# Kernel optimization log

Measured on AMD Instinct MI355X. Metric: run time of the kernel, lower is better.

## Reference

```python
import jax, jax.numpy as jnp
import numpy as np

N, K, D, H = 10000, 30, 128, 4
DH = D // H
E = N * K

def setup_inputs() -> dict:
    ks = jax.random.split(jax.random.key(0), 12)
    s = 0.05
    h = jax.random.normal(ks[0], (N, D), jnp.float32)
    e = jax.random.normal(ks[1], (E, D), jnp.float32)
    # edges grouped by source node, K neighbors each (required by the (i j) rearranges)
    src = jnp.repeat(jnp.arange(N, dtype=jnp.int32), K)
    dst = jax.random.randint(ks[2], (E,), 0, N, dtype=jnp.int32)
    edge_index = jnp.stack([src, dst], axis=0)
    return {
        'h': h, 'e': e, 'edge_index': edge_index,
        'att_w1': jax.random.normal(ks[3], (3 * D, D)) * s, 'att_b1': jnp.zeros((D,)),
        'att_w2': jax.random.normal(ks[4], (D, D)) * s,     'att_b2': jnp.zeros((D,)),
        'att_w3': jax.random.normal(ks[5], (D, H)) * s,     'att_b3': jnp.zeros((H,)),
        'node_w1': jax.random.normal(ks[6], (2 * D, D)) * s, 'node_b1': jnp.zeros((D,)),
        'node_w2': jax.random.normal(ks[7], (D, D)) * s,     'node_b2': jnp.zeros((D,)),
        'node_w3': jax.random.normal(ks[8], (D, D)) * s,     'node_b3': jnp.zeros((D,)),
        'to_h_w': jax.random.normal(ks[9], (D, D)) * s,
    }

def reference(h, e, edge_index, att_w1, att_b1, att_w2, att_b2, att_w3, att_b3,
              node_w1, node_b1, node_w2, node_b2, node_w3, node_b3, to_h_w):
    gelu = lambda x: jax.nn.gelu(x, approximate=False)  # torch nn.GELU default (erf)
    hi = h[edge_index[0]]                               # [E, D] gather
    hj = h[edge_index[1]]                               # [E, D] gather
    hi_eij_hj = jnp.concatenate([hi, e, hj], axis=-1)   # [E, 3D]
    eij_hj = jnp.concatenate([e, hj], axis=-1)          # [E, 2D]
    # attention logits per head
    w = jax.nn.relu(hi_eij_hj @ att_w1 + att_b1)
    w = jax.nn.relu(w @ att_w2 + att_b2)
    w = (w @ att_w3 + att_b3).reshape(N, K, H)          # (i j) h -> i j h
    w = w / jnp.sqrt(jnp.float32(DH))
    att = jax.nn.softmax(w, axis=1)                     # softmax over neighbors j
    # values per edge, split per head
    v = gelu(eij_hj @ node_w1 + node_b1)
    v = gelu(v @ node_w2 + node_b2)
    v = (v @ node_w3 + node_b3).reshape(N, K, H, DH)    # (i j) (h d) -> i j h d
    out = jnp.einsum('nkh,nkhd->nhd', att, v).reshape(N, D)  # weighted aggregation
    return out @ to_h_w
```

## Files before the change

kernel.cpp:

```cpp
#include <hip/hip_runtime.h>
#include <hip/hip_bf16.h>

#define N_NODES 10000
#define KNEI    30
#define DIM     128
#define EDGES   (N_NODES * KNEI)

typedef __attribute__((ext_vector_type(4))) float  f32x4;
typedef __attribute__((ext_vector_type(8))) __bf16 bf16x8;
typedef __attribute__((ext_vector_type(4))) __bf16 bf16x4;

#define OFF_AW1 0
#define OFF_AW2 49152
#define OFF_NW1 65536
#define OFF_NW2 98304
#define OFF_NW3 114688
#define OFF_TH  131072
#define TOT_TILES 288
#define YHI_BYTE_OFF (300 * 1024)

__global__ __launch_bounds__(256) void repack_all(
    const float* __restrict__ aw1, const float* __restrict__ aw2,
    const float* __restrict__ nw1, const float* __restrict__ nw2,
    const float* __restrict__ nw3, const float* __restrict__ thw,
    __bf16* __restrict__ dst) {
    int t = blockIdx.x * 256 + threadIdx.x;
    if (t >= TOT_TILES * 512) return;
    int tile = t >> 9;
    int i    = t & 7;
    int lane = (t >> 3) & 63;
    const float* src; int lt;
    if      (tile < 96)  { src = aw1; lt = tile; }
    else if (tile < 128) { src = aw2; lt = tile - 96; }
    else if (tile < 192) { src = nw1; lt = tile - 128; }
    else if (tile < 224) { src = nw2; lt = tile - 192; }
    else if (tile < 256) { src = nw3; lt = tile - 224; }
    else                 { src = thw; lt = tile - 256; }
    int nt = lt & 7;
    int kt = lt >> 3;
    int k = kt * 32 + ((lane >> 4) << 3) + i;
    int n = nt * 16 + (lane & 15);
    dst[t] = (__bf16)src[k * DIM + n];
}

__device__ __forceinline__ float gelu_f(float x) {
    float u = 0.7978845608f * (x + 0.044715f * x * x * x);
    float t = 1.f - 2.f / (__expf(2.f * u) + 1.f);
    return 0.5f * x * (1.f + t);
}

__device__ __forceinline__ bf16x4 cvt4(float4 v) {
    bf16x4 r;
    r[0] = (__bf16)v.x; r[1] = (__bf16)v.y; r[2] = (__bf16)v.z; r[3] = (__bf16)v.w;
    return r;
}

__device__ __forceinline__ void mm_lds(f32x4 acc[2], const __bf16* __restrict__ wfrag,
                                       const __bf16* x, int sx, int nkt,
                                       int wv, int lane) {
    const int mrow = lane & 15;
    const int kgrp = (lane >> 4) & 3;
#pragma unroll
    for (int kt = 0; kt < nkt; ++kt) {
        bf16x8 a = *reinterpret_cast<const bf16x8*>(wfrag + ((kt * 8 + wv) * 64 + lane) * 8);
        const int kb = kt * 32 + kgrp * 8;
#pragma unroll
        for (int mf = 0; mf < 2; ++mf) {
            bf16x8 b = *reinterpret_cast<const bf16x8*>(x + (mf * 16 + mrow) * sx + kb);
            acc[mf] = __builtin_amdgcn_mfma_f32_16x16x32_bf16(a, b, acc[mf], 0, 0, 0);
        }
    }
}

__device__ __forceinline__ void store_act(f32x4 acc[2], const float* __restrict__ bias,
                                          __bf16* y, int sy, int actmode,
                                          int wv, int lane) {
    const int mrow = lane & 15;
    const int kgrp = (lane >> 4) & 3;
    const int nb = wv * 16 + kgrp * 4;
    float b0 = bias[nb], b1 = bias[nb + 1], b2 = bias[nb + 2], b3 = bias[nb + 3];
#pragma unroll
    for (int mf = 0; mf < 2; ++mf) {
        bf16x4 pk;
        float vv[4] = {acc[mf][0] + b0, acc[mf][1] + b1, acc[mf][2] + b2, acc[mf][3] + b3};
#pragma unroll
        for (int r = 0; r < 4; ++r) {
            float v = vv[r];
            v = actmode == 0 ? fmaxf(v, 0.f) : gelu_f(v);
            pk[r] = (__bf16)v;
        }
        *reinterpret_cast<bf16x4*>(y + (mf * 16 + mrow) * sy + nb) = pk;
    }
}

#define ZERO2(A) do { A[0] = (f32x4){0.f,0.f,0.f,0.f}; A[1] = (f32x4){0.f,0.f,0.f,0.f}; } while (0)

__global__ __launch_bounds__(512) void mm128(const float* __restrict__ in,
                                             float* __restrict__ outp,
                                             const __bf16* __restrict__ wfrag,
                                             const float* __restrict__ bias) {
    __shared__ __bf16 sP[64 * 136];
    const int tid  = threadIdx.x;
    const int wv   = tid >> 6;
    const int lane = tid & 63;
    const int mrow = lane & 15;
    const int kgrp = lane >> 4;
    const int base = blockIdx.x * 64;

#pragma unroll
    for (int c = 0; c < 4; ++c) {
        int idx = c * 512 + tid;
        int m  = idx >> 5;
        int jv = idx & 31;
        int row = base + m;
        float4 v = make_float4(0.f, 0.f, 0.f, 0.f);
        if (row < N_NODES) v = *reinterpret_cast<const float4*>(in + (long)row * DIM + jv * 4);
        *reinterpret_cast<bf16x4*>(&sP[m * 136 + jv * 4]) = cvt4(v);
    }
    __syncthreads();

    f32x4 acc[4];
#pragma unroll
    for (int mf = 0; mf < 4; ++mf) acc[mf] = (f32x4){0.f, 0.f, 0.f, 0.f};
#pragma unroll
    for (int kt = 0; kt < 4; ++kt) {
        bf16x8 a = *reinterpret_cast<const bf16x8*>(wfrag + ((kt * 8 + wv) * 64 + lane) * 8);
        const int kb = kt * 32 + kgrp * 8;
#pragma unroll
        for (int mf = 0; mf < 4; ++mf) {
            bf16x8 b = *reinterpret_cast<const bf16x8*>(sP + (mf * 16 + mrow) * 136 + kb);
            acc[mf] = __builtin_amdgcn_mfma_f32_16x16x32_bf16(a, b, acc[mf], 0, 0, 0);
        }
    }
    const int nb = wv * 16 + kgrp * 4;
    float b0 = 0.f, b1 = 0.f, b2 = 0.f, b3 = 0.f;
    if (bias) { b0 = bias[nb]; b1 = bias[nb + 1]; b2 = bias[nb + 2]; b3 = bias[nb + 3]; }
#pragma unroll
    for (int mf = 0; mf < 4; ++mf) {
        int row = base + mf * 16 + mrow;
        if (row < N_NODES) {
            float4 o = make_float4(acc[mf][0] + b0, acc[mf][1] + b1,
                                   acc[mf][2] + b2, acc[mf][3] + b3);
            *reinterpret_cast<float4*>(outp + (long)row * DIM + nb) = o;
        }
    }
}

__global__ __launch_bounds__(512, 4) void gnn_fused(
    const float* __restrict__ h, const float* __restrict__ e, const int* __restrict__ eidx,
    const float* __restrict__ yhi,
    const float* __restrict__ ab2, const float* __restrict__ aw3, const float* __restrict__ ab3,
    const float* __restrict__ nb1, const float* __restrict__ nb2, const float* __restrict__ nb3,
    const __bf16* __restrict__ wp, float* __restrict__ pre_out) {

    __shared__ __bf16 S[32 * 264];
    __shared__ __bf16 Y1[32 * 136];
    __shared__ __bf16 Y2[32 * 136];
    __shared__ float  sLogW[8][32][4];
    __shared__ float  sW[32][4];

    const int tid  = threadIdx.x;
    const int wv   = tid >> 6;
    const int lane = tid & 63;
    const int mrow = lane & 15;
    const int kg   = (lane >> 4) & 3;
    const int node = blockIdx.x;
    const long ebase = (long)node * KNEI;

#pragma unroll
    for (int c = 0; c < 2; ++c) {
        int idx = c * 512 + tid;
        int m  = idx >> 5;
        int jv = idx & 31;
        float4 ev = make_float4(0.f, 0.f, 0.f, 0.f), hjv = ev;
        if (m < KNEI) {
            long ge = ebase + m;
            ev  = *reinterpret_cast<const float4*>(e + ge * DIM + jv * 4);
            int dstn = eidx[EDGES + ge];
            hjv = *reinterpret_cast<const float4*>(h + (long)dstn * DIM + jv * 4);
        }
        *reinterpret_cast<bf16x4*>(&S[m * 264 + jv * 4])       = cvt4(ev);
        *reinterpret_cast<bf16x4*>(&S[m * 264 + 128 + jv * 4]) = cvt4(hjv);
    }
    __syncthreads();

    f32x4 acc[2];

    ZERO2(acc);
    mm_lds(acc, wp + OFF_AW1 + 16384, S, 264, 8, wv, lane);
    store_act(acc, yhi + (long)node * DIM, Y1, 136, 0, wv, lane);
    __syncthreads();

    {
        ZERO2(acc);
        mm_lds(acc, wp + OFF_AW2, Y1, 136, 4, wv, lane);
        const int nb = wv * 16 + kg * 4;
        float b0 = ab2[nb], b1 = ab2[nb + 1], b2 = ab2[nb + 2], b3 = ab2[nb + 3];
        float4 w3v[4];
#pragma unroll
        for (int r = 0; r < 4; ++r)
            w3v[r] = *reinterpret_cast<const float4*>(aw3 + (nb + r) * 4);
        float lp[2][4];
#pragma unroll
        for (int mf = 0; mf < 2; ++mf) {
            lp[mf][0] = lp[mf][1] = lp[mf][2] = lp[mf][3] = 0.f;
            float vv[4] = {acc[mf][0] + b0, acc[mf][1] + b1, acc[mf][2] + b2, acc[mf][3] + b3};
#pragma unroll
            for (int r = 0; r < 4; ++r) {
                float v = fmaxf(vv[r], 0.f);
                lp[mf][0] += v * w3v[r].x;
                lp[mf][1] += v * w3v[r].y;
                lp[mf][2] += v * w3v[r].z;
                lp[mf][3] += v * w3v[r].w;
            }
        }
#pragma unroll
        for (int mf = 0; mf < 2; ++mf)
#pragma unroll
            for (int hh = 0; hh < 4; ++hh) {
                lp[mf][hh] += __shfl_xor(lp[mf][hh], 16);
                lp[mf][hh] += __shfl_xor(lp[mf][hh], 32);
            }
        if (kg == 0 && lane < 16) {
#pragma unroll
            for (int mf = 0; mf < 2; ++mf) {
                float4 o = make_float4(lp[mf][0], lp[mf][1], lp[mf][2], lp[mf][3]);
                *reinterpret_cast<float4*>(&sLogW[wv][mf * 16 + mrow][0]) = o;
            }
        }
    }
    ZERO2(acc);
    mm_lds(acc, wp + OFF_NW1, S, 264, 8, wv, lane);
    store_act(acc, nb1, Y2, 136, 1, wv, lane);
    __syncthreads();

    if (tid < 128) {
        int m = tid >> 2, hh = tid & 3;
        float s = ab3[hh];
#pragma unroll
        for (int w = 0; w < 8; ++w) s += sLogW[w][m][hh];
        sLogW[0][m][hh] = s * 0.17677669529f;
    }
    ZERO2(acc);
    mm_lds(acc, wp + OFF_NW2, Y2, 136, 4, wv, lane);
    store_act(acc, nb2, Y1, 136, 1, wv, lane);
    __syncthreads();

    ZERO2(acc);
    mm_lds(acc, wp + OFF_NW3, Y1, 136, 4, wv, lane);
    if (wv == 0 && lane < 32) {
        float4 lg = (lane < KNEI) ? *reinterpret_cast<float4*>(&sLogW[0][lane][0])
                                  : make_float4(-1e30f, -1e30f, -1e30f, -1e30f);
        float4 mx = lg;
#pragma unroll
        for (int msk = 1; msk <= 16; msk <<= 1) {
            mx.x = fmaxf(mx.x, __shfl_xor(mx.x, msk));
            mx.y = fmaxf(mx.y, __shfl_xor(mx.y, msk));
            mx.z = fmaxf(mx.z, __shfl_xor(mx.z, msk));
            mx.w = fmaxf(mx.w, __shfl_xor(mx.w, msk));
        }
        float4 ex = make_float4(__expf(lg.x - mx.x), __expf(lg.y - mx.y),
                                __expf(lg.z - mx.z), __expf(lg.w - mx.w));
        float4 sm = ex;
#pragma unroll
        for (int msk = 1; msk <= 16; msk <<= 1) {
            sm.x += __shfl_xor(sm.x, msk);
            sm.y += __shfl_xor(sm.y, msk);
            sm.z += __shfl_xor(sm.z, msk);
            sm.w += __shfl_xor(sm.w, msk);
        }
        float4 w = make_float4(ex.x / sm.x, ex.y / sm.y, ex.z / sm.z, ex.w / sm.w);
        *reinterpret_cast<float4*>(&sW[lane][0]) = w;
    }
    __syncthreads();

    {
        const int hh = wv >> 1;
        float wgt0 = sW[mrow][hh];
        float wgt1 = sW[16 + mrow][hh];
        float part[4];
#pragma unroll
        for (int r = 0; r < 4; ++r)
            part[r] = wgt0 * acc[0][r] + wgt1 * acc[1][r];
#pragma unroll
        for (int msk = 1; msk <= 8; msk <<= 1)
#pragma unroll
            for (int r = 0; r < 4; ++r)
                part[r] += __shfl_xor(part[r], msk);
        if (mrow == 0) {
            const int nb = wv * 16 + kg * 4;
            float4 o = make_float4(part[0] + nb3[nb],     part[1] + nb3[nb + 1],
                                   part[2] + nb3[nb + 2], part[3] + nb3[nb + 3]);
            *reinterpret_cast<float4*>(pre_out + (long)node * DIM + nb) = o;
        }
    }
}

extern "C" void kernel_launch(void* const* d_in, const int* in_sizes, int n_in,
                              void* d_out, int out_size, void* d_ws, size_t ws_size,
                              hipStream_t stream) {
    const float* h   = (const float*)d_in[0];
    const float* e   = (const float*)d_in[1];
    const int*   ei  = (const int*)d_in[2];
    const float* aw1 = (const float*)d_in[3];
    const float* ab1 = (const float*)d_in[4];
    const float* aw2 = (const float*)d_in[5];
    const float* ab2 = (const float*)d_in[6];
    const float* aw3 = (const float*)d_in[7];
    const float* ab3 = (const float*)d_in[8];
    const float* nw1 = (const float*)d_in[9];
    const float* nb1 = (const float*)d_in[10];
    const float* nw2 = (const float*)d_in[11];
    const float* nb2 = (const float*)d_in[12];
    const float* nw3 = (const float*)d_in[13];
    const float* nb3 = (const float*)d_in[14];
    const float* thw = (const float*)d_in[15];
    float* out = (float*)d_out;
    __bf16* wp = (__bf16*)d_ws;
    float* yhi = (float*)((char*)d_ws + YHI_BYTE_OFF);

    repack_all<<<TOT_TILES * 2, 256, 0, stream>>>(aw1, aw2, nw1, nw2, nw3, thw, wp);

    const int nblk = (N_NODES + 63) / 64;
    mm128<<<nblk, 512, 0, stream>>>(h, yhi, wp + OFF_AW1, ab1);

    gnn_fused<<<N_NODES, 512, 0, stream>>>(h, e, ei, yhi, ab2, aw3, ab3,
                                           nb1, nb2, nb3, wp, out);
    mm128<<<nblk, 512, 0, stream>>>(out, out, wp + OFF_TH, nullptr);
}
```

Measured before the change: 179.6 us.

## Merge first-layer GEMMs, split attention/value second layers across wave halves

The first-layer attention and node GEMMs now share one loop over the staged input tile, so each B fragment is loaded from LDS once and feeds both weight sets. The second layers run concurrently: waves 0-3 compute the attention layer-2 logits while waves 4-7 compute the value layer-2 GELU output into the reused S buffer. This removes one barrier stage and lets the two branches overlap instead of running back to back. The softmax is rewritten for a single wave with reciprocal instructions, and the GELU tanh form is simplified to x*sigmoid-style arithmetic with rcp. Each wave now holds more accumulators in the second layer, which may raise register pressure.

```diff
diff --git a/kernel.cpp b/kernel.cpp
--- a/kernel.cpp
+++ b/kernel.cpp
@@ -44,32 +44,15 @@
 }
 
 __device__ __forceinline__ float gelu_f(float x) {
-    float u = 0.7978845608f * (x + 0.044715f * x * x * x);
-    float t = 1.f - 2.f / (__expf(2.f * u) + 1.f);
-    return 0.5f * x * (1.f + t);
+    float y = x * fmaf(0.0713548163f, x * x, 1.5957691216f);
+    float r = __builtin_amdgcn_rcpf(__expf(y) + 1.f);
+    return x - x * r;
 }
 
 __device__ __forceinline__ bf16x4 cvt4(float4 v) {
     bf16x4 r;
     r[0] = (__bf16)v.x; r[1] = (__bf16)v.y; r[2] = (__bf16)v.z; r[3] = (__bf16)v.w;
     return r;
-}
-
-__device__ __forceinline__ void mm_lds(f32x4 acc[2], const __bf16* __restrict__ wfrag,
-                                       const __bf16* x, int sx, int nkt,
-                                       int wv, int lane) {
-    const int mrow = lane & 15;
-    const int kgrp = (lane >> 4) & 3;
-#pragma unroll
-    for (int kt = 0; kt < nkt; ++kt) {
-        bf16x8 a = *reinterpret_cast<const bf16x8*>(wfrag + ((kt * 8 + wv) * 64 + lane) * 8);
-        const int kb = kt * 32 + kgrp * 8;
-#pragma unroll
-        for (int mf = 0; mf < 2; ++mf) {
-            bf16x8 b = *reinterpret_cast<const bf16x8*>(x + (mf * 16 + mrow) * sx + kb);
-            acc[mf] = __builtin_amdgcn_mfma_f32_16x16x32_bf16(a, b, acc[mf], 0, 0, 0);
-        }
-    }
 }
 
 __device__ __forceinline__ void store_act(f32x4 acc[2], const float* __restrict__ bias,
@@ -156,7 +139,7 @@
     __shared__ __bf16 S[32 * 264];
     __shared__ __bf16 Y1[32 * 136];
     __shared__ __bf16 Y2[32 * 136];
-    __shared__ float  sLogW[8][32][4];
+    __shared__ float  sLP[4][32][4];
     __shared__ float  sW[32][4];
 
     const int tid  = threadIdx.x;
@@ -184,34 +167,66 @@
     }
     __syncthreads();
 
-    f32x4 acc[2];
-
-    ZERO2(acc);
-    mm_lds(acc, wp + OFF_AW1 + 16384, S, 264, 8, wv, lane);
-    store_act(acc, yhi + (long)node * DIM, Y1, 136, 0, wv, lane);
-    __syncthreads();
-
     {
-        ZERO2(acc);
-        mm_lds(acc, wp + OFF_AW2, Y1, 136, 4, wv, lane);
-        const int nb = wv * 16 + kg * 4;
-        float b0 = ab2[nb], b1 = ab2[nb + 1], b2 = ab2[nb + 2], b3 = ab2[nb + 3];
-        float4 w3v[4];
-#pragma unroll
-        for (int r = 0; r < 4; ++r)
-            w3v[r] = *reinterpret_cast<const float4*>(aw3 + (nb + r) * 4);
+        f32x4 aa[2], an[2];
+        ZERO2(aa); ZERO2(an);
+        const __bf16* wA = wp + OFF_AW1 + 16384;
+        const __bf16* wN = wp + OFF_NW1;
+#pragma unroll
+        for (int kt = 0; kt < 8; ++kt) {
+            const int kb = kt * 32 + kg * 8;
+            bf16x8 b0 = *reinterpret_cast<const bf16x8*>(S + mrow * 264 + kb);
+            bf16x8 b1 = *reinterpret_cast<const bf16x8*>(S + (16 + mrow) * 264 + kb);
+            bf16x8 a0 = *reinterpret_cast<const bf16x8*>(wA + ((kt * 8 + wv) * 64 + lane) * 8);
+            aa[0] = __builtin_amdgcn_mfma_f32_16x16x32_bf16(a0, b0, aa[0], 0, 0, 0);
+            aa[1] = __builtin_amdgcn_mfma_f32_16x16x32_bf16(a0, b1, aa[1], 0, 0, 0);
+            bf16x8 a1 = *reinterpret_cast<const bf16x8*>(wN + ((kt * 8 + wv) * 64 + lane) * 8);
+            an[0] = __builtin_amdgcn_mfma_f32_16x16x32_bf16(a1, b0, an[0], 0, 0, 0);
+            an[1] = __builtin_amdgcn_mfma_f32_16x16x32_bf16(a1, b1, an[1], 0, 0, 0);
+        }
+        store_act(aa, yhi + (long)node * DIM, Y1, 136, 0, wv, lane);
+        store_act(an, nb1, Y2, 136, 1, wv, lane);
+    }
+    __syncthreads();
+
+    if (wv < 4) {
+        f32x4 acc[2][2];
+        ZERO2(acc[0]); ZERO2(acc[1]);
+#pragma unroll
+        for (int kt = 0; kt < 4; ++kt) {
+            const int kb = kt * 32 + kg * 8;
+            bf16x8 b0 = *reinterpret_cast<const bf16x8*>(Y1 + mrow * 136 + kb);
+            bf16x8 b1 = *reinterpret_cast<const bf16x8*>(Y1 + (16 + mrow) * 136 + kb);
+#pragma unroll
+            for (int j = 0; j < 2; ++j) {
+                bf16x8 a = *reinterpret_cast<const bf16x8*>(wp + OFF_AW2 + (size_t)((kt * 8 + wv * 2 + j) * 64 + lane) * 8);
+                acc[j][0] = __builtin_amdgcn_mfma_f32_16x16x32_bf16(a, b0, acc[j][0], 0, 0, 0);
+                acc[j][1] = __builtin_amdgcn_mfma_f32_16x16x32_bf16(a, b1, acc[j][1], 0, 0, 0);
+            }
+        }
         float lp[2][4];
-#pragma unroll
-        for (int mf = 0; mf < 2; ++mf) {
-            lp[mf][0] = lp[mf][1] = lp[mf][2] = lp[mf][3] = 0.f;
-            float vv[4] = {acc[mf][0] + b0, acc[mf][1] + b1, acc[mf][2] + b2, acc[mf][3] + b3};
-#pragma unroll
-            for (int r = 0; r < 4; ++r) {
-                float v = fmaxf(vv[r], 0.f);
-                lp[mf][0] += v * w3v[r].x;
-                lp[mf][1] += v * w3v[r].y;
-                lp[mf][2] += v * w3v[r].z;
-                lp[mf][3] += v * w3v[r].w;
+        lp[0][0]=lp[0][1]=lp[0][2]=lp[0][3]=0.f;
+        lp[1][0]=lp[1][1]=lp[1][2]=lp[1][3]=0.f;
+#pragma unroll
+        for (int j = 0; j < 2; ++j) {
+            const int f = wv * 32 + j * 16 + kg * 4;
+            float b0 = ab2[f], b1 = ab2[f + 1], b2 = ab2[f + 2], b3 = ab2[f + 3];
+            float4 w3v[4];
+#pragma unroll
+            for (int r = 0; r < 4; ++r)
+                w3v[r] = *reinterpret_cast<const float4*>(aw3 + (f + r) * 4);
+#pragma unroll
+            for (int mf = 0; mf < 2; ++mf) {
+                float vv[4] = {acc[j][mf][0] + b0, acc[j][mf][1] + b1,
+                               acc[j][mf][2] + b2, acc[j][mf][3] + b3};
+#pragma unroll
+                for (int r = 0; r < 4; ++r) {
+                    float v = fmaxf(vv[r], 0.f);
+                    lp[mf][0] += v * w3v[r].x;
+                    lp[mf][1] += v * w3v[r].y;
+                    lp[mf][2] += v * w3v[r].z;
+                    lp[mf][3] += v * w3v[r].w;
+                }
             }
         }
 #pragma unroll
@@ -221,56 +236,75 @@
                 lp[mf][hh] += __shfl_xor(lp[mf][hh], 16);
                 lp[mf][hh] += __shfl_xor(lp[mf][hh], 32);
             }
-        if (kg == 0 && lane < 16) {
+        if (lane < 16) {
 #pragma unroll
             for (int mf = 0; mf < 2; ++mf) {
                 float4 o = make_float4(lp[mf][0], lp[mf][1], lp[mf][2], lp[mf][3]);
-                *reinterpret_cast<float4*>(&sLogW[wv][mf * 16 + mrow][0]) = o;
-            }
-        }
-    }
-    ZERO2(acc);
-    mm_lds(acc, wp + OFF_NW1, S, 264, 8, wv, lane);
-    store_act(acc, nb1, Y2, 136, 1, wv, lane);
-    __syncthreads();
-
-    if (tid < 128) {
-        int m = tid >> 2, hh = tid & 3;
-        float s = ab3[hh];
-#pragma unroll
-        for (int w = 0; w < 8; ++w) s += sLogW[w][m][hh];
-        sLogW[0][m][hh] = s * 0.17677669529f;
-    }
-    ZERO2(acc);
-    mm_lds(acc, wp + OFF_NW2, Y2, 136, 4, wv, lane);
-    store_act(acc, nb2, Y1, 136, 1, wv, lane);
-    __syncthreads();
-
-    ZERO2(acc);
-    mm_lds(acc, wp + OFF_NW3, Y1, 136, 4, wv, lane);
-    if (wv == 0 && lane < 32) {
-        float4 lg = (lane < KNEI) ? *reinterpret_cast<float4*>(&sLogW[0][lane][0])
-                                  : make_float4(-1e30f, -1e30f, -1e30f, -1e30f);
-        float4 mx = lg;
-#pragma unroll
-        for (int msk = 1; msk <= 16; msk <<= 1) {
-            mx.x = fmaxf(mx.x, __shfl_xor(mx.x, msk));
-            mx.y = fmaxf(mx.y, __shfl_xor(mx.y, msk));
-            mx.z = fmaxf(mx.z, __shfl_xor(mx.z, msk));
-            mx.w = fmaxf(mx.w, __shfl_xor(mx.w, msk));
-        }
-        float4 ex = make_float4(__expf(lg.x - mx.x), __expf(lg.y - mx.y),
-                                __expf(lg.z - mx.z), __expf(lg.w - mx.w));
-        float4 sm = ex;
-#pragma unroll
-        for (int msk = 1; msk <= 16; msk <<= 1) {
-            sm.x += __shfl_xor(sm.x, msk);
-            sm.y += __shfl_xor(sm.y, msk);
-            sm.z += __shfl_xor(sm.z, msk);
-            sm.w += __shfl_xor(sm.w, msk);
-        }
-        float4 w = make_float4(ex.x / sm.x, ex.y / sm.y, ex.z / sm.z, ex.w / sm.w);
-        *reinterpret_cast<float4*>(&sW[lane][0]) = w;
+                *reinterpret_cast<float4*>(&sLP[wv][mf * 16 + mrow][0]) = o;
+            }
+        }
+    } else {
+        const int w4 = wv - 4;
+        f32x4 acc[2][2];
+        ZERO2(acc[0]); ZERO2(acc[1]);
+#pragma unroll
+        for (int kt = 0; kt < 4; ++kt) {
+            const int kb = kt * 32 + kg * 8;
+            bf16x8 b0 = *reinterpret_cast<const bf16x8*>(Y2 + mrow * 136 + kb);
+            bf16x8 b1 = *reinterpret_cast<const bf16x8*>(Y2 + (16 + mrow) * 136 + kb);
+#pragma unroll
+            for (int j = 0; j < 2; ++j) {
+                bf16x8 a = *reinterpret_cast<const bf16x8*>(wp + OFF_NW2 + (size_t)((kt * 8 + w4 * 2 + j) * 64 + lane) * 8);
+                acc[j][0] = __builtin_amdgcn_mfma_f32_16x16x32_bf16(a, b0, acc[j][0], 0, 0, 0);
+                acc[j][1] = __builtin_amdgcn_mfma_f32_16x16x32_bf16(a, b1, acc[j][1], 0, 0, 0);
+            }
+        }
+#pragma unroll
+        for (int j = 0; j < 2; ++j) {
+            const int f = w4 * 32 + j * 16 + kg * 4;
+            float b0 = nb2[f], b1 = nb2[f + 1], b2 = nb2[f + 2], b3 = nb2[f + 3];
+#pragma unroll
+            for (int mf = 0; mf < 2; ++mf) {
+                float vv[4] = {acc[j][mf][0] + b0, acc[j][mf][1] + b1,
+                               acc[j][mf][2] + b2, acc[j][mf][3] + b3};
+                bf16x4 pk;
+#pragma unroll
+                for (int r = 0; r < 4; ++r) pk[r] = (__bf16)gelu_f(vv[r]);
+                *reinterpret_cast<bf16x4*>(S + (mf * 16 + mrow) * 136 + f) = pk;
+            }
+        }
+    }
+    __syncthreads();
+
+    if (wv == 0) {
+        const int m0 = lane >> 2, hh = lane & 3;
+        const float sc = 0.17677669529f;
+        float v0 = ab3[hh], v1 = ab3[hh];
+#pragma unroll
+        for (int w = 0; w < 4; ++w) { v0 += sLP[w][m0][hh]; v1 += sLP[w][16 + m0][hh]; }
+        v0 *= sc; v1 *= sc;
+        if (16 + m0 >= KNEI) v1 = -1e30f;
+        float mx = fmaxf(v0, v1);
+#pragma unroll
+        for (int msk = 4; msk <= 32; msk <<= 1) mx = fmaxf(mx, __shfl_xor(mx, msk));
+        float e0 = __expf(v0 - mx), e1 = __expf(v1 - mx);
+        float sm = e0 + e1;
+#pragma unroll
+        for (int msk = 4; msk <= 32; msk <<= 1) sm += __shfl_xor(sm, msk);
+        float inv = __builtin_amdgcn_rcpf(sm);
+        sW[m0][hh]      = e0 * inv;
+        sW[16 + m0][hh] = e1 * inv;
+    }
+    f32x4 v2[2];
+    ZERO2(v2);
+#pragma unroll
+    for (int kt = 0; kt < 4; ++kt) {
+        const int kb = kt * 32 + kg * 8;
+        bf16x8 b0 = *reinterpret_cast<const bf16x8*>(S + mrow * 136 + kb);
+        bf16x8 b1 = *reinterpret_cast<const bf16x8*>(S + (16 + mrow) * 136 + kb);
+        bf16x8 a = *reinterpret_cast<const bf16x8*>(wp + OFF_NW3 + (size_t)((kt * 8 + wv) * 64 + lane) * 8);
+        v2[0] = __builtin_amdgcn_mfma_f32_16x16x32_bf16(a, b0, v2[0], 0, 0, 0);
+        v2[1] = __builtin_amdgcn_mfma_f32_16x16x32_bf16(a, b1, v2[1], 0, 0, 0);
     }
     __syncthreads();
 
@@ -281,7 +315,7 @@
         float part[4];
 #pragma unroll
         for (int r = 0; r < 4; ++r)
-            part[r] = wgt0 * acc[0][r] + wgt1 * acc[1][r];
+            part[r] = wgt0 * v2[0][r] + wgt1 * v2[1][r];
 #pragma unroll
         for (int msk = 1; msk <= 8; msk <<= 1)
 #pragma unroll
```

New measurement: 153.9 us. 14.3% less time.
